# Kernel optimization log

Hardware: AMD Instinct MI355X
Metric: run time of the kernel (lower is better)

## Reference

```python
import jax, jax.numpy as jnp
import numpy as np

SPARSE_K = 8  # matches sparse_k init kwarg

def setup_inputs() -> dict:
    key = jax.random.key(0)
    k1, k2 = jax.random.split(key)
    B, N = 2, 4096
    return {
        "z_real": jax.random.normal(k1, (B, N), dtype=jnp.float32),
        "z_imag": jax.random.normal(k2, (B, N), dtype=jnp.float32),
        "resonance_strength": jnp.float32(0.1),
        "kernel_scale": jnp.float32(1.0),
        "kernel_bias": jnp.float32(0.0),
        "phase_sensitivity": jnp.float32(1.0),
    }

def reference(z_real, z_imag, resonance_strength, kernel_scale, kernel_bias, phase_sensitivity):
    B, N = z_real.shape
    # amplitude |z| and phase angle(z)
    amp = jnp.sqrt(z_real * z_real + z_imag * z_imag)          # (B, N)
    phi = jnp.arctan2(z_imag, z_real)                          # (B, N)
    # R_ij = |z_i||z_j| * |cos((phi_i - phi_j) * sens)| ** exponent
    dphi = phi[:, :, None] - phi[:, None, :]                   # (B, N, N)
    phase = jnp.abs(jnp.cos(dphi * phase_sensitivity))
    exponent = jax.nn.softplus(kernel_scale) + jax.nn.softplus(kernel_bias) + 1e-6
    phase = jnp.clip(phase, 1e-10, None) ** exponent
    R = (amp[:, :, None] * amp[:, None, :]) * phase            # (B, N, N)
    # top-k sparsify over flattened (N*N) scores, keep values >= kth-largest threshold
    total = N * N
    k_val = min(max(SPARSE_K * N, 1), total - 1)
    R_flat = R.reshape(B, total)
    thr = jax.lax.top_k(R_flat, k_val + 1)[0][:, -1:]          # (total-k_val)-th smallest
    R_sparse = jnp.where(R_flat >= thr, R_flat, 0.0).reshape(B, N, N)
    # additive mode: alpha * (R @ z), complex split into real/imag matvecs
    out_r = jnp.einsum('bij,bj->bi', R_sparse, z_real)
    out_i = jnp.einsum('bij,bj->bi', R_sparse, z_imag)
    return resonance_strength * jnp.stack([out_r, out_i], axis=-1)  # (B, N, 2) = complex out as (re, im)
```

## Files before the change

### kernel.cpp

```cpp
#include <hip/hip_runtime.h>
#include <math.h>


#define TW_N 4096
#define TW_TILE 64
#define TW_NBLK (TW_N / TW_TILE)
#define TW_TRI (TW_NBLK * (TW_NBLK + 1) / 2)
#define TW_TPB 4
#define TW_TBLK (TW_TRI / TW_TPB)
#define TW_SEGCAP (TW_TPB * TW_TILE * TW_TILE)
#define TW_NPART 8
#define TW_CAND_CAP (1 << 19)
#define TW_CBLK 64
#define TW_SBLK 128

__device__ __forceinline__ float tw_softplus(float x) {
    return fmaxf(x, 0.0f) + log1pf(expf(-fabsf(x)));
}

__device__ __forceinline__ float tw_expo(const float* ksp, const float* kbp) {
    return tw_softplus(*ksp) + tw_softplus(*kbp) + 1e-6f;
}

__device__ __forceinline__ float tw_R(float amp_i, float phi_i,
                                      float amp_j, float phi_j,
                                      float sens, float expo) {
    float dphi = phi_i - phi_j;
    float c = fabsf(cosf(dphi * sens));
    c = fmaxf(c, 1e-10f);
    float ph = powf(c, expo);
    return amp_i * amp_j * ph;
}

__device__ __forceinline__ int tw_rowstart(int bi) {
    return bi * TW_NBLK - ((bi * (bi - 1)) >> 1);
}
__device__ __forceinline__ void tw_decode(int tt, int& bi, int& bj) {
    const float A = (float)(2 * TW_NBLK + 1);
    float disc = A * A - 8.0f * (float)tt;
    int b = (int)((A - sqrtf(disc)) * 0.5f);
    if (b < 0) b = 0;
    if (b > TW_NBLK - 1) b = TW_NBLK - 1;
    while (b + 1 <= TW_NBLK - 1 && tw_rowstart(b + 1) <= tt) ++b;
    while (b > 0 && tw_rowstart(b) > tt) --b;
    bi = b;
    bj = b + (tt - tw_rowstart(b));
}

template <int NB>
__device__ void tw_scan_dev(const unsigned* __restrict__ h, unsigned Kp_in,
                            unsigned& bin_out, unsigned& kp_out) {
    __shared__ unsigned ps_[256];
    __shared__ unsigned shb_, shk_;
    constexpr int CHUNK = NB / 256;
    const int t = threadIdx.x;
    __syncthreads();
    unsigned s = 0;
    for (int k = 0; k < CHUNK; ++k) s += h[NB - 1 - (t * CHUNK + k)];
    ps_[t] = s;
    __syncthreads();
    for (int off = 1; off < 256; off <<= 1) {
        unsigned v = (t >= off) ? ps_[t - off] : 0u;
        __syncthreads();
        ps_[t] += v;
        __syncthreads();
    }
    unsigned excl = (t == 0) ? 0u : ps_[t - 1];
    if (excl < Kp_in && Kp_in <= ps_[t]) {
        unsigned run = excl;
        for (int k = 0; k < CHUNK; ++k) {
            int bin = NB - 1 - (t * CHUNK + k);
            unsigned c = h[bin];
            if (run + c >= Kp_in) { shb_ = (unsigned)bin; shk_ = Kp_in - run; break; }
            run += c;
        }
    }
    __syncthreads();
    bin_out = shb_; kp_out = shk_;
}

__device__ float tw_wmin_dev(const unsigned* __restrict__ histp, int b, int B, unsigned K) {
    __shared__ unsigned ps_[256];
    __shared__ unsigned shm_;
    const int t = threadIdx.x;
    unsigned s = 0;
    for (int k = 0; k < 8; ++k) {
        int bin = 2047 - (t * 8 + k);
        for (int p = 0; p < TW_NPART; ++p)
            s += histp[((size_t)p * B + b) * 2048 + bin];
    }
    ps_[t] = s;
    __syncthreads();
    for (int off = 1; off < 256; off <<= 1) {
        unsigned v = (t >= off) ? ps_[t - off] : 0u;
        __syncthreads();
        ps_[t] += v;
        __syncthreads();
    }
    unsigned excl = (t == 0) ? 0u : ps_[t - 1];
    if (excl < K && K <= ps_[t]) {
        unsigned run = excl;
        for (int k = 0; k < 8; ++k) {
            int bin = 2047 - (t * 8 + k);
            unsigned c = 0;
            for (int p = 0; p < TW_NPART; ++p)
                c += histp[((size_t)p * B + b) * 2048 + bin];
            if (run + c >= K) {
                int mb = bin - 2; if (mb < 0) mb = 0;
                shm_ = (unsigned)mb << 20;
                break;
            }
            run += c;
        }
    }
    __syncthreads();
    return __uint_as_float(shm_);
}

__global__ void tw_init(const float* __restrict__ zr, const float* __restrict__ zi,
                        float2* __restrict__ jfast, float4* __restrict__ jexact,
                        unsigned* __restrict__ zero_base, int zero_words,
                        float* __restrict__ out, int out_words,
                        const float* ksp, const float* kbp, int total) {
    const int idx = blockIdx.x * blockDim.x + threadIdx.x;
    const int stride = gridDim.x * blockDim.x;
    for (int k = idx; k < zero_words; k += stride) zero_base[k] = 0u;
    for (int k = idx; k < out_words; k += stride) out[k] = 0.0f;
    if (idx < total) {
        float r = zr[idx], m = zi[idx];
        float amp = sqrtf(r * r + m * m);
        float phi = atan2f(m, r);
        jexact[idx] = make_float4(amp, phi, r, m);
        float e = tw_expo(ksp, kbp);
        jfast[idx] = make_float2(powf(amp, 1.0f / e), phi);
    }
}

__global__ void tw_histW(const float2* __restrict__ jf, unsigned* __restrict__ histp,
                         const float* __restrict__ sensp, int N, int B) {
    __shared__ float s_jv[TW_TILE], s_jp[TW_TILE];
    __shared__ unsigned lh[2048 * 4];
    const int b = blockIdx.y, tid = threadIdx.x;
    const int jj = tid & 63, r0 = tid >> 6;
    const int rep = tid & 3;
    for (int k = tid; k < 2048 * 4; k += 256) lh[k] = 0u;
    const float sens = *sensp;
    int bi, bj;
    tw_decode(blockIdx.x * TW_TPB, bi, bj);
    for (int s = 0; s < TW_TPB; ++s) {
        __syncthreads();
        if (tid < TW_TILE) {
            float2 w = jf[b * N + bj * TW_TILE + tid];
            s_jv[tid] = w.x; s_jp[tid] = w.y;
        }
        float vi[16], ph[16];
#pragma unroll
        for (int k = 0; k < 16; ++k) {
            float2 v = jf[b * N + bi * TW_TILE + r0 + (k << 2)];
            vi[k] = v.x; ph[k] = v.y;
        }
        __syncthreads();
        const float vj = s_jv[jj], pj = s_jp[jj];
        const unsigned inc = (bi == bj) ? 1u : 2u;
#pragma unroll
        for (int k = 0; k < 16; ++k) {
            float w = vi[k] * vj * fabsf(__cosf((ph[k] - pj) * sens));
            atomicAdd(&lh[((__float_as_uint(w) >> 20) << 2) + rep], inc);
        }
        ++bj;
        if (bj >= TW_NBLK) { ++bi; bj = bi; }
    }
    __syncthreads();
    unsigned* hp = histp + ((size_t)(blockIdx.x & (TW_NPART - 1)) * B + b) * 2048;
    const int rot = (int)((blockIdx.x * 191u + b * 977u) & 2047u);
    for (int kk = tid; kk < 2048; kk += 256) {
        int k = (kk + rot) & 2047;
        unsigned v = lh[k * 4] + lh[k * 4 + 1] + lh[k * 4 + 2] + lh[k * 4 + 3];
        if (v) atomicAdd(&hp[k], v);
    }
}

__global__ void tw_collectW(const float2* __restrict__ jf, const unsigned* __restrict__ histp,
                            unsigned* __restrict__ seg, unsigned* __restrict__ cnt,
                            const float* __restrict__ sensp, int N, int B, unsigned K) {
    __shared__ float s_jv[TW_TILE], s_jp[TW_TILE];
    __shared__ unsigned cn;
    const int b = blockIdx.y, tid = threadIdx.x;
    const int jj = tid & 63, r0 = tid >> 6;
    const float wmin = tw_wmin_dev(histp, b, B, K);
    if (tid == 0) cn = 0u;
    const float sens = *sensp;
    const int gid = b * TW_TBLK + blockIdx.x;
    unsigned* sg = seg + (size_t)gid * TW_SEGCAP;
    int bi, bj;
    tw_decode(blockIdx.x * TW_TPB, bi, bj);
    for (int s = 0; s < TW_TPB; ++s) {
        __syncthreads();
        if (tid < TW_TILE) {
            float2 w = jf[b * N + bj * TW_TILE + tid];
            s_jv[tid] = w.x; s_jp[tid] = w.y;
        }
        float vi[16], ph[16];
#pragma unroll
        for (int k = 0; k < 16; ++k) {
            float2 v = jf[b * N + bi * TW_TILE + r0 + (k << 2)];
            vi[k] = v.x; ph[k] = v.y;
        }
        __syncthreads();
        const float vj = s_jv[jj], pj = s_jp[jj];
        const unsigned ib = (unsigned)(bi * TW_TILE);
        const unsigned jg = (unsigned)(bj * TW_TILE) + (unsigned)jj;
#pragma unroll
        for (int k = 0; k < 16; ++k) {
            float w = vi[k] * vj * fabsf(__cosf((ph[k] - pj) * sens));
            if (w >= wmin) {
                unsigned p = atomicAdd(&cn, 1u);
                sg[p] = ((ib + (unsigned)(r0 + (k << 2))) << 12) | jg;
            }
        }
        ++bj;
        if (bj >= TW_NBLK) { ++bi; bj = bi; }
    }
    __syncthreads();
    if (tid == 0) cnt[gid] = cn;
}

__device__ __forceinline__ unsigned tw_w(unsigned pij) {
    return ((pij >> 18) == ((pij >> 6) & 63u)) ? 1u : 2u;
}

__global__ void tw_gexact(const unsigned* __restrict__ seg, const unsigned* __restrict__ cnt,
                          unsigned* __restrict__ cand_idx, float* __restrict__ cand_val,
                          const float4* __restrict__ jdata, unsigned* __restrict__ histA,
                          unsigned* __restrict__ ccount,
                          const float* ksp, const float* kbp, const float* sensp,
                          int N, int perb, int cap) {
    __shared__ unsigned lh[4096];
    __shared__ unsigned red[256];
    const int b = blockIdx.y, tid = threadIdx.x;
    for (int k = tid; k < 4096; k += 256) lh[k] = 0u;
    unsigned partial = 0;
    for (int k = tid; k < (int)blockIdx.x; k += 256) partial += cnt[b * perb + k];
    red[tid] = partial;
    __syncthreads();
    for (int off = 128; off; off >>= 1) {
        if (tid < off) red[tid] += red[tid + off];
        __syncthreads();
    }
    const unsigned dbase = red[0];
    const int gid = b * perb + blockIdx.x;
    const unsigned n = cnt[gid];
    if (blockIdx.x == perb - 1 && tid == 0) ccount[b] = dbase + n;
    const unsigned* src = seg + (size_t)gid * TW_SEGCAP;
    const float sens = *sensp;
    const float expo = tw_expo(ksp, kbp);
    __syncthreads();
    for (unsigned k = tid; k < n; k += 256) {
        unsigned pij = src[k];
        unsigned d = dbase + k;
        if (d >= (unsigned)cap) continue;
        const unsigned i = pij >> 12, j = pij & 4095u;
        float4 di = jdata[b * N + i];
        float4 dj = jdata[b * N + j];
        float val = tw_R(di.x, di.y, dj.x, dj.y, sens, expo);
        cand_idx[(size_t)b * cap + d] = pij;
        cand_val[(size_t)b * cap + d] = val;
        atomicAdd(&lh[__float_as_uint(val) >> 20], tw_w(pij));
    }
    __syncthreads();
    for (int k = tid; k < 4096; k += 256) {
        unsigned v = lh[k];
        if (v) atomicAdd(&histA[b * 4096 + k], v);
    }
}

__global__ void tw_chist1f(const float* __restrict__ cand_val, const unsigned* __restrict__ cand_idx,
                           const unsigned* __restrict__ ccount, const unsigned* __restrict__ histA,
                           unsigned* __restrict__ histB, unsigned K, int cap) {
    __shared__ unsigned lh[4096];
    const int b = blockIdx.y, tid = threadIdx.x;
    unsigned binA, KpA;
    tw_scan_dev<4096>(histA + (size_t)b * 4096, K, binA, KpA);
    for (int k = tid; k < 4096; k += 256) lh[k] = 0u;
    unsigned nb = ccount[b]; if (nb > (unsigned)cap) nb = (unsigned)cap;
    const float* cv = cand_val + (size_t)b * cap;
    const unsigned* ci = cand_idx + (size_t)b * cap;
    __syncthreads();
    const unsigned stride = gridDim.x * 256;
    for (unsigned idx = blockIdx.x * 256 + tid; idx < nb; idx += stride) {
        unsigned bits = __float_as_uint(cv[idx]);
        if ((bits >> 20) == binA) atomicAdd(&lh[(bits >> 8) & 0xFFFu], tw_w(ci[idx]));
    }
    __syncthreads();
    for (int k = tid; k < 4096; k += 256) {
        unsigned v = lh[k];
        if (v) atomicAdd(&histB[b * 4096 + k], v);
    }
}

__global__ void tw_chist2f(const float* __restrict__ cand_val, const unsigned* __restrict__ cand_idx,
                           const unsigned* __restrict__ ccount, const unsigned* __restrict__ histA,
                           const unsigned* __restrict__ histB, unsigned* __restrict__ histC,
                           unsigned K, int cap) {
    __shared__ unsigned lh[256];
    const int b = blockIdx.y, tid = threadIdx.x;
    unsigned binA, KpA, binB, KpB;
    tw_scan_dev<4096>(histA + (size_t)b * 4096, K, binA, KpA);
    tw_scan_dev<4096>(histB + (size_t)b * 4096, KpA, binB, KpB);
    if (tid < 256) lh[tid] = 0u;
    unsigned nb = ccount[b]; if (nb > (unsigned)cap) nb = (unsigned)cap;
    const unsigned pf24 = (binA << 12) | binB;
    const float* cv = cand_val + (size_t)b * cap;
    const unsigned* ci = cand_idx + (size_t)b * cap;
    __syncthreads();
    const unsigned stride = gridDim.x * 256;
    for (unsigned idx = blockIdx.x * 256 + tid; idx < nb; idx += stride) {
        unsigned bits = __float_as_uint(cv[idx]);
        if ((bits >> 8) == pf24) atomicAdd(&lh[bits & 0xFFu], tw_w(ci[idx]));
    }
    __syncthreads();
    if (tid < 256) {
        unsigned v = lh[tid];
        if (v) atomicAdd(&histC[b * 256 + tid], v);
    }
}

__global__ void tw_scatterf(const float* __restrict__ cand_val, const unsigned* __restrict__ cand_idx,
                            const unsigned* __restrict__ ccount, const unsigned* __restrict__ histA,
                            const unsigned* __restrict__ histB, const unsigned* __restrict__ histC,
                            const float4* __restrict__ jdata, const float* alphap,
                            float* __restrict__ out, unsigned K, int N, int cap) {
    const int b = blockIdx.y;
    unsigned binA, KpA, binB, KpB, binC, KpC;
    tw_scan_dev<4096>(histA + (size_t)b * 4096, K, binA, KpA);
    tw_scan_dev<4096>(histB + (size_t)b * 4096, KpA, binB, KpB);
    tw_scan_dev<256>(histC + (size_t)b * 256, KpB, binC, KpC);
    const float T = __uint_as_float((binA << 20) | (binB << 8) | binC);
    unsigned nb = ccount[b]; if (nb > (unsigned)cap) nb = (unsigned)cap;
    const float alpha = *alphap;
    const unsigned stride = gridDim.x * 256;
    for (unsigned idx = blockIdx.x * 256 + threadIdx.x; idx < nb; idx += stride) {
        const float v = cand_val[(size_t)b * cap + idx];
        if (v < T) continue;
        const unsigned pij = cand_idx[(size_t)b * cap + idx];
        const unsigned i = pij >> 12, j = pij & 4095u;
        float4 dj = jdata[b * N + j];
        atomicAdd(&out[(size_t)(b * N + i) * 2 + 0], alpha * v * dj.z);
        atomicAdd(&out[(size_t)(b * N + i) * 2 + 1], alpha * v * dj.w);
        if ((pij >> 18) != ((pij >> 6) & 63u)) {
            float4 di = jdata[b * N + i];
            atomicAdd(&out[(size_t)(b * N + j) * 2 + 0], alpha * v * di.z);
            atomicAdd(&out[(size_t)(b * N + j) * 2 + 1], alpha * v * di.w);
        }
    }
}


__global__ void tw_precompute(const float* __restrict__ zr, const float* __restrict__ zi,
                              float4* __restrict__ jdata, unsigned* __restrict__ state,
                              int total, int B, unsigned K) {
    int idx = blockIdx.x * blockDim.x + threadIdx.x;
    if (idx < total) {
        float r = zr[idx], m = zi[idx];
        float amp = sqrtf(r * r + m * m);
        float phi = atan2f(m, r);
        jdata[idx] = make_float4(amp, phi, r, m);
    }
    if (idx < B) { state[idx * 2 + 0] = 0u; state[idx * 2 + 1] = K; }
}

template <int PASS>
__global__ void tw_hist(const float4* __restrict__ jdata, unsigned* __restrict__ hist,
                        const unsigned* __restrict__ state,
                        const float* ksp, const float* kbp, const float* sensp, int N) {
    constexpr int NB = (PASS == 3) ? 256 : 4096;
    __shared__ float sa[256], sphi[256];
    __shared__ unsigned lh[NB];
    const int b = blockIdx.z;
    const int i = blockIdx.x * 256 + threadIdx.x;
    const int j0 = blockIdx.y * 256;

    for (int k = threadIdx.x; k < NB; k += 256) lh[k] = 0u;

    float4 mine = jdata[b * N + i];
    float amp_i = mine.x, phi_i = mine.y;
    float4 jd = jdata[b * N + j0 + threadIdx.x];
    sa[threadIdx.x] = jd.x; sphi[threadIdx.x] = jd.y;

    const float sens = *sensp;
    const float expo = tw_expo(ksp, kbp);
    unsigned pf = 0;
    if (PASS > 1) pf = state[b * 2 + 0];
    __syncthreads();

    for (int j = 0; j < 256; ++j) {
        float R = tw_R(amp_i, phi_i, sa[j], sphi[j], sens, expo);
        unsigned bits = __float_as_uint(R);
        if (PASS == 1) {
            atomicAdd(&lh[bits >> 20], 1u);
        } else if (PASS == 2) {
            if ((bits >> 20) == (pf >> 20)) atomicAdd(&lh[(bits >> 8) & 0xFFFu], 1u);
        } else {
            if ((bits >> 8) == (pf >> 8)) atomicAdd(&lh[bits & 0xFFu], 1u);
        }
    }
    __syncthreads();
    for (int k = threadIdx.x; k < NB; k += 256) {
        unsigned v = lh[k];
        if (v) atomicAdd(&hist[b * NB + k], v);
    }
}

template <int NB, int SHIFT>
__global__ void tw_scan(const unsigned* __restrict__ hist, unsigned* __restrict__ state,
                        float* __restrict__ thr, int B) {
    __shared__ unsigned ps[256];
    constexpr int CHUNK = NB / 256;
    const int t = threadIdx.x;
    for (int b = 0; b < B; ++b) {
        const unsigned* h = hist + b * NB;
        unsigned prefix = state[b * 2 + 0];
        unsigned Kp     = state[b * 2 + 1];
        unsigned s = 0;
        for (int k = 0; k < CHUNK; ++k) {
            int bin = NB - 1 - (t * CHUNK + k);
            s += h[bin];
        }
        ps[t] = s;
        __syncthreads();
        for (int off = 1; off < 256; off <<= 1) {
            unsigned v = (t >= off) ? ps[t - off] : 0u;
            __syncthreads();
            ps[t] += v;
            __syncthreads();
        }
        unsigned excl = (t == 0) ? 0u : ps[t - 1];
        unsigned incl = ps[t];
        if (excl < Kp && Kp <= incl) {
            unsigned run = excl;
            for (int k = 0; k < CHUNK; ++k) {
                int bin = NB - 1 - (t * CHUNK + k);
                unsigned c = h[bin];
                if (run + c >= Kp) {
                    unsigned npf = prefix | ((unsigned)bin << SHIFT);
                    state[b * 2 + 0] = npf;
                    state[b * 2 + 1] = Kp - run;
                    if (SHIFT == 0) thr[b] = __uint_as_float(npf);
                    break;
                }
                run += c;
            }
        }
        __syncthreads();
    }
}

__global__ void tw_matvec(const float4* __restrict__ jdata, const float* __restrict__ thr,
                          const float* alphap, const float* ksp, const float* kbp,
                          const float* sensp, float* __restrict__ out, int N) {
    const int b = blockIdx.y;
    const int wid = threadIdx.x >> 6;
    const int lane = threadIdx.x & 63;
    const int i = blockIdx.x * 4 + wid;

    float4 mine = jdata[b * N + i];
    float amp_i = mine.x, phi_i = mine.y;
    const float sens = *sensp;
    const float expo = tw_expo(ksp, kbp);
    const float T = thr[b];
    const float alpha = *alphap;

    float ar = 0.0f, ai = 0.0f;
    for (int j = lane; j < N; j += 64) {
        float4 jd = jdata[b * N + j];
        float R = tw_R(amp_i, phi_i, jd.x, jd.y, sens, expo);
        if (R >= T) { ar += R * jd.z; ai += R * jd.w; }
    }
    for (int off = 32; off; off >>= 1) {
        ar += __shfl_down(ar, off);
        ai += __shfl_down(ai, off);
    }
    if (lane == 0) {
        out[(b * N + i) * 2 + 0] = alpha * ar;
        out[(b * N + i) * 2 + 1] = alpha * ai;
    }
}


static inline size_t tw_align(size_t x) { return (x + 255) & ~(size_t)255; }

extern "C" void kernel_launch(void* const* d_in, const int* in_sizes, int n_in,
                              void* d_out, int out_size, void* d_ws, size_t ws_size,
                              hipStream_t stream) {
    const float* zr    = (const float*)d_in[0];
    const float* zi    = (const float*)d_in[1];
    const float* alpha = (const float*)d_in[2];
    const float* ks    = (const float*)d_in[3];
    const float* kb    = (const float*)d_in[4];
    const float* sens  = (const float*)d_in[5];
    float* out = (float*)d_out;

    const int N = TW_N;
    const int B = in_sizes[0] / N;
    const int total = B * N;

    long long tot2 = (long long)N * N;
    long long kv = (long long)8 * N;
    if (kv < 1) kv = 1;
    if (kv > tot2 - 1) kv = tot2 - 1;
    const unsigned K = (unsigned)(kv + 1);

    char* ws = (char*)d_ws;

    size_t o_hP     = 0;
    size_t o_hA     = o_hP + (size_t)TW_NPART * B * 2048 * sizeof(unsigned);
    size_t o_hB     = o_hA + (size_t)B * 4096 * sizeof(unsigned);
    size_t o_hC     = o_hB + (size_t)B * 4096 * sizeof(unsigned);
    size_t o_cnt    = o_hC + (size_t)B * 256 * sizeof(unsigned);
    size_t o_ccount = o_cnt + (size_t)B * TW_TBLK * sizeof(unsigned);
    size_t o_zero_end = o_ccount + (size_t)B * sizeof(unsigned);
    size_t o_jfast  = tw_align(o_zero_end);
    size_t o_jexact = tw_align(o_jfast + (size_t)B * N * sizeof(float2));
    size_t o_cidx   = tw_align(o_jexact + (size_t)B * N * sizeof(float4));
    size_t o_cval   = tw_align(o_cidx + (size_t)B * TW_CAND_CAP * sizeof(unsigned));
    size_t o_seg    = tw_align(o_cval + (size_t)B * TW_CAND_CAP * sizeof(float));
    size_t o_end    = o_seg + (size_t)B * TW_TBLK * TW_SEGCAP * sizeof(unsigned);

    if (ws_size >= o_end) {
        unsigned* hP     = (unsigned*)(ws + o_hP);
        unsigned* hA     = (unsigned*)(ws + o_hA);
        unsigned* hB     = (unsigned*)(ws + o_hB);
        unsigned* hC     = (unsigned*)(ws + o_hC);
        unsigned* cnt    = (unsigned*)(ws + o_cnt);
        unsigned* ccount = (unsigned*)(ws + o_ccount);
        float2*   jfast  = (float2*)(ws + o_jfast);
        float4*   jexact = (float4*)(ws + o_jexact);
        unsigned* cidx   = (unsigned*)(ws + o_cidx);
        float*    cval   = (float*)(ws + o_cval);
        unsigned* seg    = (unsigned*)(ws + o_seg);

        const int zero_words = (int)(o_zero_end / sizeof(unsigned));
        tw_init<<<128, 256, 0, stream>>>(zr, zi, jfast, jexact, (unsigned*)ws, zero_words,
                                         out, out_size, ks, kb, total);

        dim3 tgrid(TW_TBLK, B);
        tw_histW<<<tgrid, 256, 0, stream>>>(jfast, hP, sens, N, B);
        tw_collectW<<<tgrid, 256, 0, stream>>>(jfast, hP, seg, cnt, sens, N, B, K);
        tw_gexact<<<tgrid, 256, 0, stream>>>(seg, cnt, cidx, cval, jexact, hA, ccount,
                                             ks, kb, sens, N, TW_TBLK, TW_CAND_CAP);
        tw_chist1f<<<dim3(TW_CBLK, B), 256, 0, stream>>>(cval, cidx, ccount, hA, hB, K, TW_CAND_CAP);
        tw_chist2f<<<dim3(TW_CBLK, B), 256, 0, stream>>>(cval, cidx, ccount, hA, hB, hC, K, TW_CAND_CAP);
        tw_scatterf<<<dim3(TW_SBLK, B), 256, 0, stream>>>(cval, cidx, ccount, hA, hB, hC,
                                                          jexact, alpha, out, K, N, TW_CAND_CAP);
        return;
    }

    size_t l_jdata = 0;
    size_t l_h1 = l_jdata + (size_t)B * N * sizeof(float4);
    size_t l_h2 = l_h1 + (size_t)B * 4096 * sizeof(unsigned);
    size_t l_h3 = l_h2 + (size_t)B * 4096 * sizeof(unsigned);
    size_t l_state = l_h3 + (size_t)B * 256 * sizeof(unsigned);
    size_t l_thr = l_state + (size_t)B * 2 * sizeof(unsigned);
    size_t l_end = l_thr + (size_t)B * sizeof(float);

    float4* jdata = (float4*)(ws + l_jdata);
    unsigned* h1 = (unsigned*)(ws + l_h1);
    unsigned* h2 = (unsigned*)(ws + l_h2);
    unsigned* h3 = (unsigned*)(ws + l_h3);
    unsigned* state = (unsigned*)(ws + l_state);
    float* thr = (float*)(ws + l_thr);

    (void)hipMemsetAsync(ws + l_h1, 0, l_end - l_h1, stream);

    tw_precompute<<<(total + 255) / 256, 256, 0, stream>>>(zr, zi, jdata, state, total, B, K);

    dim3 hgrid(N / 256, N / 256, B);
    tw_hist<1><<<hgrid, 256, 0, stream>>>(jdata, h1, state, ks, kb, sens, N);
    tw_scan<4096, 20><<<1, 256, 0, stream>>>(h1, state, thr, B);
    tw_hist<2><<<hgrid, 256, 0, stream>>>(jdata, h2, state, ks, kb, sens, N);
    tw_scan<4096, 8><<<1, 256, 0, stream>>>(h2, state, thr, B);
    tw_hist<3><<<hgrid, 256, 0, stream>>>(jdata, h3, state, ks, kb, sens, N);
    tw_scan<256, 0><<<1, 256, 0, stream>>>(h3, state, thr, B);

    tw_matvec<<<dim3(N / 4, B), 256, 0, stream>>>(jdata, thr, alpha, ks, kb, sens, out, N);
}
```

Before: 109.8 us.

## Fuse all top-k pipeline stages into one cooperative kernel with grid syncs

Replaces the seven separate kernel launches (init, histogram, collect, exact gather, three refinement histograms and scatter) with a single cooperative megakernel that separates the phases with grid.sync(). This is meant to remove per-launch overhead and inter-kernel gaps. Tiles per block go from 4 to 5 so the grid (416 blocks) fits co-resident on the device. The old multi-kernel path stays as a fallback if occupancy is too low or the cooperative launch fails. Larger shared memory and launch bounds may limit occupancy, and the grid barriers add their own cost.

```diff
diff --git a/kernel.cpp b/kernel.cpp
--- a/kernel.cpp
+++ b/kernel.cpp
@@ -1,12 +1,15 @@
 #include <hip/hip_runtime.h>
+#include <hip/hip_cooperative_groups.h>
 #include <math.h>
+
+namespace cg = cooperative_groups;
 
 
 #define TW_N 4096
 #define TW_TILE 64
 #define TW_NBLK (TW_N / TW_TILE)
 #define TW_TRI (TW_NBLK * (TW_NBLK + 1) / 2)
-#define TW_TPB 4
+#define TW_TPB 5
 #define TW_TBLK (TW_TRI / TW_TPB)
 #define TW_SEGCAP (TW_TPB * TW_TILE * TW_TILE)
 #define TW_NPART 8
@@ -116,6 +119,244 @@
     __syncthreads();
     return __uint_as_float(shm_);
 }
+
+__device__ __forceinline__ unsigned tw_w(unsigned pij) {
+    return ((pij >> 18) == ((pij >> 6) & 63u)) ? 1u : 2u;
+}
+
+__global__ void __launch_bounds__(256, 4)
+tw_mega(const float* zr, const float* zi,
+        const float* alphap, const float* ksp, const float* kbp, const float* sensp,
+        float* out, int out_words,
+        unsigned* hP, unsigned* hA, unsigned* hB, unsigned* hC,
+        unsigned* cnt, unsigned* ccount,
+        float2* jfast, float4* jexact,
+        unsigned* cidx, float* cval, unsigned* seg,
+        unsigned* zero_base, int zero_words,
+        int N, int B, int total, unsigned K) {
+    cg::grid_group grid = cg::this_grid();
+    __shared__ unsigned s_lh[2048 * 4];
+    __shared__ float s_jv[TW_TILE], s_jp[TW_TILE];
+    __shared__ unsigned s_cn;
+
+    const int tid = threadIdx.x;
+    const int b = blockIdx.y;
+    const int bx = blockIdx.x;
+
+    {
+        const int bid = blockIdx.y * gridDim.x + blockIdx.x;
+        const int idx0 = bid * 256 + tid;
+        const int stride = gridDim.x * gridDim.y * 256;
+        for (int k = idx0; k < zero_words; k += stride) zero_base[k] = 0u;
+        for (int k = idx0; k < out_words; k += stride) out[k] = 0.0f;
+        const float e = tw_expo(ksp, kbp);
+        for (int k = idx0; k < total; k += stride) {
+            float r = zr[k], m = zi[k];
+            float amp = sqrtf(r * r + m * m);
+            float phi = atan2f(m, r);
+            jexact[k] = make_float4(amp, phi, r, m);
+            jfast[k] = make_float2(powf(amp, 1.0f / e), phi);
+        }
+    }
+    __threadfence();
+    grid.sync();
+
+    {
+        for (int k = tid; k < 2048 * 4; k += 256) s_lh[k] = 0u;
+        const float sens = *sensp;
+        const int jj = tid & 63, r0 = tid >> 6, rep = tid & 3;
+        int bi, bj;
+        tw_decode(bx * TW_TPB, bi, bj);
+        for (int s = 0; s < TW_TPB; ++s) {
+            __syncthreads();
+            if (tid < TW_TILE) {
+                float2 w = jfast[b * N + bj * TW_TILE + tid];
+                s_jv[tid] = w.x; s_jp[tid] = w.y;
+            }
+            float vi[16], ph[16];
+#pragma unroll
+            for (int k = 0; k < 16; ++k) {
+                float2 v = jfast[b * N + bi * TW_TILE + r0 + (k << 2)];
+                vi[k] = v.x; ph[k] = v.y;
+            }
+            __syncthreads();
+            const float vj = s_jv[jj], pj = s_jp[jj];
+            const unsigned inc = (bi == bj) ? 1u : 2u;
+#pragma unroll
+            for (int k = 0; k < 16; ++k) {
+                float w = vi[k] * vj * fabsf(__cosf((ph[k] - pj) * sens));
+                atomicAdd(&s_lh[((__float_as_uint(w) >> 20) << 2) + rep], inc);
+            }
+            ++bj;
+            if (bj >= TW_NBLK) { ++bi; bj = bi; }
+        }
+        __syncthreads();
+        unsigned* hp = hP + ((size_t)(bx & (TW_NPART - 1)) * B + b) * 2048;
+        const int rot = (int)((bx * 191u + b * 977u) & 2047u);
+        for (int kk = tid; kk < 2048; kk += 256) {
+            int k = (kk + rot) & 2047;
+            unsigned v = s_lh[k * 4] + s_lh[k * 4 + 1] + s_lh[k * 4 + 2] + s_lh[k * 4 + 3];
+            if (v) atomicAdd(&hp[k], v);
+        }
+    }
+    __threadfence();
+    grid.sync();
+
+    {
+        const float wmin = tw_wmin_dev(hP, b, B, K);
+        if (tid == 0) s_cn = 0u;
+        const float sens = *sensp;
+        const int jj = tid & 63, r0 = tid >> 6;
+        const int gid = b * TW_TBLK + bx;
+        unsigned* sg = seg + (size_t)gid * TW_SEGCAP;
+        int bi, bj;
+        tw_decode(bx * TW_TPB, bi, bj);
+        for (int s = 0; s < TW_TPB; ++s) {
+            __syncthreads();
+            if (tid < TW_TILE) {
+                float2 w = jfast[b * N + bj * TW_TILE + tid];
+                s_jv[tid] = w.x; s_jp[tid] = w.y;
+            }
+            float vi[16], ph[16];
+#pragma unroll
+            for (int k = 0; k < 16; ++k) {
+                float2 v = jfast[b * N + bi * TW_TILE + r0 + (k << 2)];
+                vi[k] = v.x; ph[k] = v.y;
+            }
+            __syncthreads();
+            const float vj = s_jv[jj], pj = s_jp[jj];
+            const unsigned ib = (unsigned)(bi * TW_TILE);
+            const unsigned jg = (unsigned)(bj * TW_TILE) + (unsigned)jj;
+#pragma unroll
+            for (int k = 0; k < 16; ++k) {
+                float w = vi[k] * vj * fabsf(__cosf((ph[k] - pj) * sens));
+                if (w >= wmin) {
+                    unsigned p = atomicAdd(&s_cn, 1u);
+                    sg[p] = ((ib + (unsigned)(r0 + (k << 2))) << 12) | jg;
+                }
+            }
+            ++bj;
+            if (bj >= TW_NBLK) { ++bi; bj = bi; }
+        }
+        __syncthreads();
+        if (tid == 0) cnt[gid] = s_cn;
+    }
+    __threadfence();
+    grid.sync();
+
+    {
+        unsigned* lh = s_lh;
+        unsigned* red = s_lh + 4096;
+        for (int k = tid; k < 4096; k += 256) lh[k] = 0u;
+        unsigned partial = 0;
+        for (int k = tid; k < bx; k += 256) partial += cnt[b * TW_TBLK + k];
+        red[tid] = partial;
+        __syncthreads();
+        for (int off = 128; off; off >>= 1) {
+            if (tid < off) red[tid] += red[tid + off];
+            __syncthreads();
+        }
+        const unsigned dbase = red[0];
+        const int gid = b * TW_TBLK + bx;
+        const unsigned n = cnt[gid];
+        if (bx == TW_TBLK - 1 && tid == 0) ccount[b] = dbase + n;
+        const unsigned* src = seg + (size_t)gid * TW_SEGCAP;
+        const float sens = *sensp;
+        const float expo = tw_expo(ksp, kbp);
+        __syncthreads();
+        for (unsigned k = tid; k < n; k += 256) {
+            unsigned pij = src[k];
+            unsigned d = dbase + k;
+            if (d >= (unsigned)TW_CAND_CAP) continue;
+            const unsigned i = pij >> 12, j = pij & 4095u;
+            float4 di = jexact[b * N + i];
+            float4 dj = jexact[b * N + j];
+            float val = tw_R(di.x, di.y, dj.x, dj.y, sens, expo);
+            cidx[(size_t)b * TW_CAND_CAP + d] = pij;
+            cval[(size_t)b * TW_CAND_CAP + d] = val;
+            atomicAdd(&lh[__float_as_uint(val) >> 20], tw_w(pij));
+        }
+        __syncthreads();
+        for (int k = tid; k < 4096; k += 256) {
+            unsigned v = lh[k];
+            if (v) atomicAdd(&hA[b * 4096 + k], v);
+        }
+    }
+    __threadfence();
+    grid.sync();
+
+    {
+        unsigned binA, KpA;
+        tw_scan_dev<4096>(hA + (size_t)b * 4096, K, binA, KpA);
+        for (int k = tid; k < 4096; k += 256) s_lh[k] = 0u;
+        unsigned nb = ccount[b]; if (nb > (unsigned)TW_CAND_CAP) nb = (unsigned)TW_CAND_CAP;
+        const float* cv = cval + (size_t)b * TW_CAND_CAP;
+        const unsigned* ci = cidx + (size_t)b * TW_CAND_CAP;
+        __syncthreads();
+        const unsigned stride = gridDim.x * 256;
+        for (unsigned idx = bx * 256 + tid; idx < nb; idx += stride) {
+            unsigned bits = __float_as_uint(cv[idx]);
+            if ((bits >> 20) == binA) atomicAdd(&s_lh[(bits >> 8) & 0xFFFu], tw_w(ci[idx]));
+        }
+        __syncthreads();
+        for (int k = tid; k < 4096; k += 256) {
+            unsigned v = s_lh[k];
+            if (v) atomicAdd(&hB[b * 4096 + k], v);
+        }
+    }
+    __threadfence();
+    grid.sync();
+
+    {
+        unsigned binA, KpA, binB, KpB;
+        tw_scan_dev<4096>(hA + (size_t)b * 4096, K, binA, KpA);
+        tw_scan_dev<4096>(hB + (size_t)b * 4096, KpA, binB, KpB);
+        if (tid < 256) s_lh[tid] = 0u;
+        unsigned nb = ccount[b]; if (nb > (unsigned)TW_CAND_CAP) nb = (unsigned)TW_CAND_CAP;
+        const unsigned pf24 = (binA << 12) | binB;
+        const float* cv = cval + (size_t)b * TW_CAND_CAP;
+        const unsigned* ci = cidx + (size_t)b * TW_CAND_CAP;
+        __syncthreads();
+        const unsigned stride = gridDim.x * 256;
+        for (unsigned idx = bx * 256 + tid; idx < nb; idx += stride) {
+            unsigned bits = __float_as_uint(cv[idx]);
+            if ((bits >> 8) == pf24) atomicAdd(&s_lh[bits & 0xFFu], tw_w(ci[idx]));
+        }
+        __syncthreads();
+        if (tid < 256) {
+            unsigned v = s_lh[tid];
+            if (v) atomicAdd(&hC[b * 256 + tid], v);
+        }
+    }
+    __threadfence();
+    grid.sync();
+
+    {
+        unsigned binA, KpA, binB, KpB, binC, KpC;
+        tw_scan_dev<4096>(hA + (size_t)b * 4096, K, binA, KpA);
+        tw_scan_dev<4096>(hB + (size_t)b * 4096, KpA, binB, KpB);
+        tw_scan_dev<256>(hC + (size_t)b * 256, KpB, binC, KpC);
+        const float T = __uint_as_float((binA << 20) | (binB << 8) | binC);
+        unsigned nb = ccount[b]; if (nb > (unsigned)TW_CAND_CAP) nb = (unsigned)TW_CAND_CAP;
+        const float alpha = *alphap;
+        const unsigned stride = gridDim.x * 256;
+        for (unsigned idx = bx * 256 + tid; idx < nb; idx += stride) {
+            const float v = cval[(size_t)b * TW_CAND_CAP + idx];
+            if (v < T) continue;
+            const unsigned pij = cidx[(size_t)b * TW_CAND_CAP + idx];
+            const unsigned i = pij >> 12, j = pij & 4095u;
+            float4 dj = jexact[b * N + j];
+            atomicAdd(&out[(size_t)(b * N + i) * 2 + 0], alpha * v * dj.z);
+            atomicAdd(&out[(size_t)(b * N + i) * 2 + 1], alpha * v * dj.w);
+            if ((pij >> 18) != ((pij >> 6) & 63u)) {
+                float4 di = jexact[b * N + i];
+                atomicAdd(&out[(size_t)(b * N + j) * 2 + 0], alpha * v * di.z);
+                atomicAdd(&out[(size_t)(b * N + j) * 2 + 1], alpha * v * di.w);
+            }
+        }
+    }
+}
+
 
 __global__ void tw_init(const float* __restrict__ zr, const float* __restrict__ zi,
                         float2* __restrict__ jfast, float4* __restrict__ jexact,
@@ -223,10 +464,6 @@
     }
     __syncthreads();
     if (tid == 0) cnt[gid] = cn;
-}
-
-__device__ __forceinline__ unsigned tw_w(unsigned pij) {
-    return ((pij >> 18) == ((pij >> 6) & 63u)) ? 1u : 2u;
 }
 
 __global__ void tw_gexact(const unsigned* __restrict__ seg, const unsigned* __restrict__ cnt,
@@ -539,7 +776,37 @@
         float*    cval   = (float*)(ws + o_cval);
         unsigned* seg    = (unsigned*)(ws + o_seg);
 
-        const int zero_words = (int)(o_zero_end / sizeof(unsigned));
+        int zero_words = (int)(o_zero_end / sizeof(unsigned));
+        int out_words  = out_size;
+        unsigned* zbase = (unsigned*)ws;
+        int Ni = N, Bi = B, Ti = total;
+        unsigned Ku = K;
+
+        static int coop_max = -1;
+        if (coop_max < 0) {
+            int perCU = 0, nCU = 0, dev = 0;
+            (void)hipGetDevice(&dev);
+            if (hipOccupancyMaxActiveBlocksPerMultiprocessor(
+                    &perCU, (const void*)tw_mega, 256, 0) != hipSuccess) perCU = 0;
+            if (hipDeviceGetAttribute(&nCU, hipDeviceAttributeMultiprocessorCount,
+                                      dev) != hipSuccess) nCU = 0;
+            coop_max = perCU * nCU;
+        }
+        if (coop_max >= TW_TBLK * B) {
+            void* kargs[] = {
+                (void*)&zr, (void*)&zi, (void*)&alpha, (void*)&ks, (void*)&kb, (void*)&sens,
+                (void*)&out, (void*)&out_words,
+                (void*)&hP, (void*)&hA, (void*)&hB, (void*)&hC,
+                (void*)&cnt, (void*)&ccount, (void*)&jfast, (void*)&jexact,
+                (void*)&cidx, (void*)&cval, (void*)&seg, (void*)&zbase,
+                (void*)&zero_words, (void*)&Ni, (void*)&Bi, (void*)&Ti, (void*)&Ku
+            };
+            dim3 g(TW_TBLK, B), blk(256, 1, 1);
+            if (hipLaunchCooperativeKernel((const void*)tw_mega, g, blk,
+                                           kargs, 0, stream) == hipSuccess)
+                return;
+        }
+
         tw_init<<<128, 256, 0, stream>>>(zr, zi, jfast, jexact, (unsigned*)ws, zero_words,
                                          out, out_size, ks, kb, total);
 
```

After: 107.9 us. About the same (-1.8%).

## Fuse multi-kernel top-k pipeline into one persistent kernel with grid barriers

Applied to the files above, without the earlier changes.

Adds a persistent kernel that runs the histogram, candidate collection, two-level radix threshold refinement and scatter-accumulate matvec as phases of a single launch, separated by software grid barriers per batch. Candidates keep their exact values in a block-local segment, so the separate exact recomputation and global candidate compaction passes are dropped. The point is to remove kernel launch gaps and intermediate global round-trips. In exchange it needs every block co-resident, checked through an occupancy query, and it relies on spin-wait barriers. It also changes tiles-per-block to 5, which also affects the fallback path.

```diff
diff --git a/kernel.cpp b/kernel.cpp
--- a/kernel.cpp
+++ b/kernel.cpp
@@ -6,7 +6,7 @@
 #define TW_TILE 64
 #define TW_NBLK (TW_N / TW_TILE)
 #define TW_TRI (TW_NBLK * (TW_NBLK + 1) / 2)
-#define TW_TPB 4
+#define TW_TPB 5
 #define TW_TBLK (TW_TRI / TW_TPB)
 #define TW_SEGCAP (TW_TPB * TW_TILE * TW_TILE)
 #define TW_NPART 8
@@ -45,6 +45,25 @@
     while (b > 0 && tw_rowstart(b) > tt) --b;
     bi = b;
     bj = b + (tt - tw_rowstart(b));
+}
+
+__device__ __forceinline__ void tw_gbar(unsigned* bar, unsigned target, unsigned gen) {
+    __syncthreads();
+    __builtin_amdgcn_fence(__ATOMIC_RELEASE, "agent");
+    if (threadIdx.x == 0) {
+        unsigned v = __hip_atomic_fetch_add(&bar[0], 1u, __ATOMIC_RELAXED,
+                                            __HIP_MEMORY_SCOPE_AGENT);
+        if (v + 1u == target) {
+            __hip_atomic_store(&bar[1], gen, __ATOMIC_RELAXED,
+                               __HIP_MEMORY_SCOPE_AGENT);
+        } else {
+            while (__hip_atomic_load(&bar[1], __ATOMIC_RELAXED,
+                                     __HIP_MEMORY_SCOPE_AGENT) < gen)
+                __builtin_amdgcn_s_sleep(2);
+        }
+    }
+    __syncthreads();
+    __builtin_amdgcn_fence(__ATOMIC_ACQUIRE, "agent");
 }
 
 template <int NB>
@@ -116,6 +135,191 @@
     __syncthreads();
     return __uint_as_float(shm_);
 }
+
+__device__ __forceinline__ unsigned tw_w(unsigned pij) {
+    return ((pij >> 18) == ((pij >> 6) & 63u)) ? 1u : 2u;
+}
+
+__global__ void __launch_bounds__(256, 4)
+tw_p3(const float* zr, const float* zi,
+      const float* alphap, const float* ksp, const float* kbp, const float* sensp,
+      float* out, int out_words,
+      unsigned* hP, unsigned* h16c, unsigned* h16, unsigned* hLoc, unsigned* hLo,
+      unsigned* bar, uint2* seg, int N, int B, unsigned K) {
+    __shared__ unsigned s_lh[2048 * 4];
+    __shared__ float s_iv[TW_TILE], s_ia[TW_TILE], s_ip[TW_TILE];
+    __shared__ float s_jv[TW_TILE], s_ja[TW_TILE], s_jp[TW_TILE];
+    __shared__ unsigned s_cn;
+
+    const int tid = threadIdx.x;
+    const int b = blockIdx.y;
+    const int bx = blockIdx.x;
+    const int jj = tid & 63, r0 = tid >> 6, rep = tid & 3;
+    const float sens = *sensp;
+    const float expo = tw_expo(ksp, kbp);
+    const float inv_e = 1.0f / expo;
+    unsigned* mybar = bar + b * 2;
+    uint2* sg = seg + (size_t)(b * TW_TBLK + bx) * TW_SEGCAP;
+
+    {
+        const int bid = b * gridDim.x + bx;
+        const int gs = gridDim.x * gridDim.y * 256;
+        for (int k = bid * 256 + tid; k < out_words; k += gs) out[k] = 0.0f;
+        for (int k = tid; k < 2048 * 4; k += 256) s_lh[k] = 0u;
+        int bi, bj;
+        tw_decode(bx * TW_TPB, bi, bj);
+        int cur = -1;
+        for (int s = 0; s < TW_TPB; ++s) {
+            __syncthreads();
+            if (tid < TW_TILE) {
+                int g = b * N + bj * TW_TILE + tid;
+                float r = zr[g], m = zi[g];
+                float amp = sqrtf(r * r + m * m);
+                s_jv[tid] = powf(amp, inv_e);
+                s_jp[tid] = atan2f(m, r);
+            } else if (tid < 2 * TW_TILE && bi != cur) {
+                int t = tid - TW_TILE;
+                int g = b * N + bi * TW_TILE + t;
+                float r = zr[g], m = zi[g];
+                float amp = sqrtf(r * r + m * m);
+                s_iv[t] = powf(amp, inv_e);
+                s_ip[t] = atan2f(m, r);
+            }
+            cur = bi;
+            __syncthreads();
+            float vi[16], ph[16];
+#pragma unroll
+            for (int k = 0; k < 16; ++k) {
+                int il = r0 + (k << 2);
+                vi[k] = s_iv[il]; ph[k] = s_ip[il];
+            }
+            const float vj = s_jv[jj], pj = s_jp[jj];
+            const unsigned inc = (bi == bj) ? 1u : 2u;
+#pragma unroll
+            for (int k = 0; k < 16; ++k) {
+                float w = vi[k] * vj * fabsf(__cosf((ph[k] - pj) * sens));
+                atomicAdd(&s_lh[((__float_as_uint(w) >> 20) << 2) + rep], inc);
+            }
+            ++bj;
+            if (bj >= TW_NBLK) { ++bi; bj = bi; }
+        }
+        __syncthreads();
+        unsigned* hp = hP + ((size_t)(bx & (TW_NPART - 1)) * B + b) * 2048;
+        const int rot = (int)((bx * 191u + b * 977u) & 2047u);
+        for (int kk = tid; kk < 2048; kk += 256) {
+            int k = (kk + rot) & 2047;
+            unsigned v = s_lh[k * 4] + s_lh[k * 4 + 1] + s_lh[k * 4 + 2] + s_lh[k * 4 + 3];
+            if (v) atomicAdd(&hp[k], v);
+        }
+    }
+    tw_gbar(mybar, TW_TBLK * 1u, 1u);
+
+    {
+        const float wmin = tw_wmin_dev(hP, b, B, K);
+        if (tid == 0) s_cn = 0u;
+        for (int k = tid; k < 1024; k += 256) s_lh[k] = 0u;
+        int bi, bj;
+        tw_decode(bx * TW_TPB, bi, bj);
+        int cur = -1;
+        for (int s = 0; s < TW_TPB; ++s) {
+            __syncthreads();
+            if (tid < TW_TILE) {
+                int g = b * N + bj * TW_TILE + tid;
+                float r = zr[g], m = zi[g];
+                float amp = sqrtf(r * r + m * m);
+                s_ja[tid] = amp;
+                s_jv[tid] = powf(amp, inv_e);
+                s_jp[tid] = atan2f(m, r);
+            } else if (tid < 2 * TW_TILE && bi != cur) {
+                int t = tid - TW_TILE;
+                int g = b * N + bi * TW_TILE + t;
+                float r = zr[g], m = zi[g];
+                float amp = sqrtf(r * r + m * m);
+                s_ia[t] = amp;
+                s_iv[t] = powf(amp, inv_e);
+                s_ip[t] = atan2f(m, r);
+            }
+            cur = bi;
+            __syncthreads();
+            const float vj = s_jv[jj], pj = s_jp[jj], aj = s_ja[jj];
+            const unsigned ib = (unsigned)(bi * TW_TILE);
+            const unsigned jg = (unsigned)(bj * TW_TILE) + (unsigned)jj;
+            const unsigned wg = (bi == bj) ? 1u : 2u;
+#pragma unroll
+            for (int k = 0; k < 16; ++k) {
+                const int il = r0 + (k << 2);
+                float w = s_iv[il] * vj * fabsf(__cosf((s_ip[il] - pj) * sens));
+                if (w >= wmin) {
+                    float val = tw_R(s_ia[il], s_ip[il], aj, pj, sens, expo);
+                    unsigned bits = __float_as_uint(val);
+                    unsigned pij = ((ib + (unsigned)il) << 12) | jg;
+                    unsigned p = atomicAdd(&s_cn, 1u);
+                    sg[p] = make_uint2(pij, bits);
+                    atomicAdd(&h16[((size_t)b << 16) + (bits >> 16)], wg);
+                    atomicAdd(&s_lh[((bits >> 24) << 2) + rep], wg);
+                }
+            }
+            ++bj;
+            if (bj >= TW_NBLK) { ++bi; bj = bi; }
+        }
+        __syncthreads();
+        if (tid < 256) {
+            unsigned v = s_lh[tid * 4] + s_lh[tid * 4 + 1] + s_lh[tid * 4 + 2] + s_lh[tid * 4 + 3];
+            if (v) atomicAdd(&h16c[b * 256 + tid], v);
+        }
+    }
+    tw_gbar(mybar, TW_TBLK * 2u, 2u);
+
+    {
+        unsigned c8, Kp1, f8, Kp2;
+        tw_scan_dev<256>(h16c + b * 256, K, c8, Kp1);
+        tw_scan_dev<256>(h16 + ((size_t)b << 16) + (c8 << 8), Kp1, f8, Kp2);
+        const unsigned bin16 = (c8 << 8) | f8;
+        for (int k = tid; k < 1024; k += 256) s_lh[k] = 0u;
+        const unsigned cn = s_cn;
+        __syncthreads();
+        for (unsigned k = tid; k < cn; k += 256) {
+            uint2 u = sg[k];
+            if ((u.y >> 16) == bin16) {
+                unsigned wg = tw_w(u.x);
+                atomicAdd(&hLo[((size_t)b << 16) + (u.y & 0xFFFFu)], wg);
+                atomicAdd(&s_lh[(((u.y >> 8) & 0xFFu) << 2) + rep], wg);
+            }
+        }
+        __syncthreads();
+        if (tid < 256) {
+            unsigned v = s_lh[tid * 4] + s_lh[tid * 4 + 1] + s_lh[tid * 4 + 2] + s_lh[tid * 4 + 3];
+            if (v) atomicAdd(&hLoc[b * 256 + tid], v);
+        }
+    }
+    tw_gbar(mybar, TW_TBLK * 3u, 3u);
+
+    {
+        unsigned c8, Kp1, f8, Kp2, cL, Kp3, fL, Kp4;
+        tw_scan_dev<256>(h16c + b * 256, K, c8, Kp1);
+        tw_scan_dev<256>(h16 + ((size_t)b << 16) + (c8 << 8), Kp1, f8, Kp2);
+        tw_scan_dev<256>(hLoc + b * 256, Kp2, cL, Kp3);
+        tw_scan_dev<256>(hLo + ((size_t)b << 16) + (cL << 8), Kp3, fL, Kp4);
+        const float T = __uint_as_float((((c8 << 8) | f8) << 16) | (cL << 8) | fL);
+        const float alpha = *alphap;
+        const unsigned cn = s_cn;
+        for (unsigned k = tid; k < cn; k += 256) {
+            uint2 u = sg[k];
+            const float v = __uint_as_float(u.y);
+            if (v < T) continue;
+            const unsigned i = u.x >> 12, j = u.x & 4095u;
+            float zjr = zr[b * N + j], zji = zi[b * N + j];
+            atomicAdd(&out[(size_t)(b * N + i) * 2 + 0], alpha * v * zjr);
+            atomicAdd(&out[(size_t)(b * N + i) * 2 + 1], alpha * v * zji);
+            if ((u.x >> 18) != ((u.x >> 6) & 63u)) {
+                float zir = zr[b * N + i], zii = zi[b * N + i];
+                atomicAdd(&out[(size_t)(b * N + j) * 2 + 0], alpha * v * zir);
+                atomicAdd(&out[(size_t)(b * N + j) * 2 + 1], alpha * v * zii);
+            }
+        }
+    }
+}
+
 
 __global__ void tw_init(const float* __restrict__ zr, const float* __restrict__ zi,
                         float2* __restrict__ jfast, float4* __restrict__ jexact,
@@ -223,10 +427,6 @@
     }
     __syncthreads();
     if (tid == 0) cnt[gid] = cn;
-}
-
-__device__ __forceinline__ unsigned tw_w(unsigned pij) {
-    return ((pij >> 18) == ((pij >> 6) & 63u)) ? 1u : 2u;
 }
 
 __global__ void tw_gexact(const unsigned* __restrict__ seg, const unsigned* __restrict__ cnt,
@@ -512,6 +712,41 @@
 
     char* ws = (char*)d_ws;
 
+    size_t p_hP   = 0;
+    size_t p_h16c = p_hP + (size_t)TW_NPART * B * 2048 * sizeof(unsigned);
+    size_t p_h16  = p_h16c + (size_t)B * 256 * sizeof(unsigned);
+    size_t p_hLoc = p_h16 + (size_t)B * 65536 * sizeof(unsigned);
+    size_t p_hLo  = p_hLoc + (size_t)B * 256 * sizeof(unsigned);
+    size_t p_bar  = p_hLo + (size_t)B * 65536 * sizeof(unsigned);
+    size_t p_zend = p_bar + (size_t)B * 2 * sizeof(unsigned);
+    size_t p_seg  = tw_align(p_zend);
+    size_t p_end  = p_seg + (size_t)B * TW_TBLK * TW_SEGCAP * sizeof(uint2);
+
+    static int persist_max = -1;
+    if (persist_max < 0) {
+        int perCU = 0, nCU = 0, dev = 0;
+        (void)hipGetDevice(&dev);
+        if (hipOccupancyMaxActiveBlocksPerMultiprocessor(
+                &perCU, (const void*)tw_p3, 256, 0) != hipSuccess) perCU = 0;
+        if (hipDeviceGetAttribute(&nCU, hipDeviceAttributeMultiprocessorCount,
+                                  dev) != hipSuccess) nCU = 0;
+        persist_max = perCU * nCU;
+    }
+    if (ws_size >= p_end && persist_max >= TW_TBLK * B) {
+        unsigned* hP   = (unsigned*)(ws + p_hP);
+        unsigned* h16c = (unsigned*)(ws + p_h16c);
+        unsigned* h16  = (unsigned*)(ws + p_h16);
+        unsigned* hLoc = (unsigned*)(ws + p_hLoc);
+        unsigned* hLo  = (unsigned*)(ws + p_hLo);
+        unsigned* bar  = (unsigned*)(ws + p_bar);
+        uint2*    seg  = (uint2*)(ws + p_seg);
+        (void)hipMemsetAsync(ws, 0, p_zend, stream);
+        tw_p3<<<dim3(TW_TBLK, B), 256, 0, stream>>>(
+            zr, zi, alpha, ks, kb, sens, out, out_size,
+            hP, h16c, h16, hLoc, hLo, bar, seg, N, B, K);
+        return;
+    }
+
     size_t o_hP     = 0;
     size_t o_hA     = o_hP + (size_t)TW_NPART * B * 2048 * sizeof(unsigned);
     size_t o_hB     = o_hA + (size_t)B * 4096 * sizeof(unsigned);
```

Result: no change. 107.7 us (-1.9%).
